# Kernel tuning notes

Measured on AMD Instinct MI355X. Metric: run time of the kernel, lower is better.

The kernel has to match this reference:

```python
import jax, jax.numpy as jnp
import numpy as np
from math import factorial as _f

MAX_L = 2
NUM_CHANNELS = 64
B, N, C = 4, 1024, 64


def _cg_coeff(l1, m1, l2, m2, L, M):
    # Standard real Clebsch-Gordan coefficient <l1 m1 l2 m2 | L M> (Condon-Shortley)
    if m1 + m2 != M or not (abs(l1 - l2) <= L <= l1 + l2):
        return 0.0
    pre = ((2 * L + 1) * _f(L + l1 - l2) * _f(L - l1 + l2) * _f(l1 + l2 - L) / _f(l1 + l2 + L + 1)) ** 0.5
    pre *= (_f(L + M) * _f(L - M) * _f(l1 - m1) * _f(l1 + m1) * _f(l2 - m2) * _f(l2 + m2)) ** 0.5
    s = 0.0
    for k in range(0, l1 + l2 - L + 1):
        dens = [k, l1 + l2 - L - k, l1 - m1 - k, l2 + m2 - k, L - l2 + m1 + k, L - l1 - m2 + k]
        if any(d < 0 for d in dens):
            continue
        term = (-1.0) ** k
        for d in dens:
            term /= _f(d)
        s += term
    return pre * s


def _cg_tensor(l1, l2, L):
    # dense CG block [2l1+1, 2l2+1, 2L+1]
    T = np.zeros((2 * l1 + 1, 2 * l2 + 1, 2 * L + 1), np.float32)
    for i, m1 in enumerate(range(-l1, l1 + 1)):
        for j, m2 in enumerate(range(-l2, l2 + 1)):
            for k, M in enumerate(range(-L, L + 1)):
                T[i, j, k] = _cg_coeff(l1, m1, l2, m2, L, M)
    return jnp.asarray(T)


# precompute small CG blocks once (tiny, static)
_CG = {(l1, l2, L): _cg_tensor(l1, l2, L)
       for l1 in range(MAX_L + 1) for l2 in range(MAX_L + 1)
       for L in range(MAX_L + 1) if abs(l1 - l2) <= L <= l1 + l2}


def setup_inputs() -> dict:
    key = jax.random.key(0)
    ks = jax.random.split(key, 7)
    inp = {}
    for l, k in zip(range(MAX_L + 1), ks[:3]):
        inp[f"v{l}"] = jax.random.normal(k, (B, N, 2 * l + 1, C), jnp.float32)
    for l, k in zip(range(MAX_L + 1), ks[3:6]):
        inp[f"s{l}"] = jax.random.normal(k, (B, N, N, 2 * l + 1, 1), jnp.float32)
    inp["conn"] = jax.random.randint(ks[6], (B, N, N), 0, 2, jnp.int32)
    return inp


def reference(v0, v1, v2, s0, s1, s2, conn):
    v = [v0, v1, v2]
    sph = [s0, s1, s2]
    # sphx.parts[l] = einsum('bijmc->bimc', sph.parts[l]) : sum over neighbor index j
    sx = [jnp.einsum('bijmc->bimc', s) for s in sph]
    adj = conn.astype(v0.dtype)  # [B,N,N] gather mask (Rmask1)

    # CGproduct(vertices, sphx): for each output degree L, concat all (l1,l2) fragments
    cg_parts = []
    for L in range(MAX_L + 1):
        frags = []
        for l1 in range(MAX_L + 1):
            for l2 in range(MAX_L + 1):
                if abs(l1 - l2) <= L <= l1 + l2:
                    # [B,N,2L+1,C*1]
                    o = jnp.einsum('bnic,bnjd,ijk->bnkcd', v[l1], sx[l2], _CG[(l1, l2, L)])
                    frags.append(o.reshape(o.shape[0], o.shape[1], 2 * L + 1, -1))
        cg_parts.append(jnp.concatenate(frags, axis=-1))

    # message passing: sum-gather over connected neighbors
    mp = [jnp.einsum('bnm,bmkc->bnkc', adj, p) for p in cg_parts]

    # per-l normalization: divide by (2l+1)*||part||_F / num_channels
    normed = []
    for L, p in enumerate(mp):
        nf = (2 * L + 1) * jnp.linalg.norm(p)
        normed.append(p / (nf / NUM_CHANNELS))

    # flatten (m, channel) per degree and concat for a single output array
    return jnp.concatenate([p.reshape(p.shape[0], p.shape[1], -1) for p in normed], axis=-1)
```

## Files before the change

### kernel.cpp

```cpp
#include <hip/hip_runtime.h>
#include <math.h>

typedef __attribute__((ext_vector_type(8))) short short8;
typedef __attribute__((ext_vector_type(4))) float f32x4;

#define B_   4
#define N_   1024
#define FTOT 3264
#define FPAD 3328

#define WS_SS   0
#define WS_CG   256
#define WS_SX   4096
#define WS_ABF  151552
#define WS_PT   8540160

__device__ __forceinline__ unsigned short f2bf(float x) {
  union { float f; unsigned u; } v; v.f = x;
  unsigned r = v.u + 0x7FFFu + ((v.u >> 16) & 1u);
  return (unsigned short)(r >> 16);
}

__device__ __forceinline__ void gload16(const void* gp, void* lp) {
  __builtin_amdgcn_global_load_lds((const __attribute__((address_space(1))) unsigned int*)gp,
                                   (__attribute__((address_space(3))) unsigned int*)lp, 16, 0, 0);
}

__device__ __forceinline__ float wave_sum(float v) {
#pragma unroll
  for (int off = 32; off > 0; off >>= 1) v += __shfl_down(v, off, 64);
  return v;
}

__device__ double dfact(int n) { double r = 1.0; for (int i = 2; i <= n; ++i) r *= (double)i; return r; }

__device__ float cg_coeff(int l1, int m1, int l2, int m2, int L, int M) {
  if (m1 + m2 != M) return 0.f;
  int dl = l1 - l2; if (dl < 0) dl = -dl;
  if (L < dl || L > l1 + l2) return 0.f;
  double pre = sqrt((double)(2*L+1) * dfact(L+l1-l2) * dfact(L-l1+l2) * dfact(l1+l2-L) / dfact(l1+l2+L+1));
  pre *= sqrt(dfact(L+M)*dfact(L-M)*dfact(l1-m1)*dfact(l1+m1)*dfact(l2-m2)*dfact(l2+m2));
  double s = 0.0;
  for (int k = 0; k <= l1 + l2 - L; ++k) {
    int d1 = l1+l2-L-k, d2 = l1-m1-k, d3 = l2+m2-k, d4 = L-l2+m1+k, d5 = L-l1-m2+k;
    if (d1 < 0 || d2 < 0 || d3 < 0 || d4 < 0 || d5 < 0) continue;
    double t = (k & 1) ? -1.0 : 1.0;
    t /= dfact(k)*dfact(d1)*dfact(d2)*dfact(d3)*dfact(d4)*dfact(d5);
    s += t;
  }
  return (float)(pre * s);
}

__device__ const int t_l1[15]  = {0,1,2, 0,1,1,1,2,2, 0,1,1,2,2,2};
__device__ const int t_l2[15]  = {0,1,2, 1,0,1,2,1,2, 2,1,2,0,1,2};
__device__ const int t_L [15]  = {0,0,0, 1,1,1,1,1,1, 2,2,2,2,2,2};
__device__ const int t_off[16] = {0,1,10, 35,44,53,80,125,170, 245,270,315,390,415,490, 615};

__device__ const int d_l1[3][6]  = {{0,1,2,0,0,0},{0,1,1,1,2,2},{0,1,1,2,2,2}};
__device__ const int d_l2[3][6]  = {{0,1,2,0,0,0},{1,0,1,2,1,2},{2,1,2,0,1,2}};
__device__ const int d_off[3][6] = {{0,1,10,0,0,0},{35,44,53,80,125,170},{245,270,315,390,415,490}};
__device__ const int d_rb[3] = {0, 1, 4};


__global__ void k_init(float* ss, float* cg) {
  int tid = threadIdx.x;
  if (tid < 4) ss[tid] = 0.f;
  if (tid >= 615) return;
  int t = 0;
  while (t < 14 && tid >= t_off[t+1]) ++t;
  int local = tid - t_off[t];
  int l1 = t_l1[t], l2 = t_l2[t], L = t_L[t];
  int nk = 2*L+1, n2 = 2*l2+1;
  int k = local % nk; int rest = local / nk;
  int j = rest % n2;  int i = rest / n2;
  cg[tid] = cg_coeff(l1, i - l1, l2, j - l2, L, k - L);
}

__global__ __launch_bounds__(256) void k_sx(const float* __restrict__ s0p, const float* __restrict__ s1p,
                                            const float* __restrict__ s2p, float* __restrict__ sx) {
  __shared__ float red[9][256];
  const int bn = blockIdx.x;
  const int tid = threadIdx.x;
  const float* p0 = s0p + (size_t)bn * 1024;
  const float* p1 = s1p + (size_t)bn * 3072;
  const float* p2 = s2p + (size_t)bn * 5120;
  float a0 = 0.f;
  for (int i = tid; i < 1024; i += 256) a0 += p0[i];
  float b0 = 0.f, b1 = 0.f, b2 = 0.f;
  for (int i = tid; i < 3072; i += 768) { b0 += p1[i]; b1 += p1[i+256]; b2 += p1[i+512]; }
  float c0=0.f,c1=0.f,c2=0.f,c3=0.f,c4=0.f;
  for (int i = tid; i < 5120; i += 1280) {
    c0 += p2[i]; c1 += p2[i+256]; c2 += p2[i+512]; c3 += p2[i+768]; c4 += p2[i+1024];
  }
  red[0][tid] = a0;
  const int r3 = tid % 3;
  red[1 + r3][tid]        = b0;
  red[1 + (r3+1)%3][tid]  = b1;
  red[1 + (r3+2)%3][tid]  = b2;
  const int r5 = tid % 5;
  red[4 + r5][tid]        = c0;
  red[4 + (r5+1)%5][tid]  = c1;
  red[4 + (r5+2)%5][tid]  = c2;
  red[4 + (r5+3)%5][tid]  = c3;
  red[4 + (r5+4)%5][tid]  = c4;
  __syncthreads();
  for (int s = 128; s > 0; s >>= 1) {
    if (tid < s) {
#pragma unroll
      for (int r = 0; r < 9; ++r) red[r][tid] += red[r][tid + s];
    }
    __syncthreads();
  }
  if (tid < 9) sx[(size_t)bn * 9 + tid] = red[tid][0];
}

__global__ __launch_bounds__(256) void k_adj(const int* __restrict__ conn, unsigned short* __restrict__ Abf) {
  const int idx  = blockIdx.x * 256 + threadIdx.x;
  const int lane = idx & 63;
  const int w    = (idx >> 6) & 2047;
  const int b    = idx >> 17;
  const int nt16 = w >> 5;
  const int ks   = w & 31;
  const int l16  = lane & 15, quad = lane >> 4;
  const int n    = nt16 * 16 + l16;
  const int m8   = ks * 32 + quad * 8;
  const int4* src = (const int4*)(conn + ((size_t)(b * 1024 + n) * 1024 + m8));
  int4 c0 = src[0], c1 = src[1];
  short8 o;
  o[0] = f2bf((float)c0.x); o[1] = f2bf((float)c0.y);
  o[2] = f2bf((float)c0.z); o[3] = f2bf((float)c0.w);
  o[4] = f2bf((float)c1.x); o[5] = f2bf((float)c1.y);
  o[6] = f2bf((float)c1.z); o[7] = f2bf((float)c1.w);
  const int nt = n >> 7, nr = n & 127;
  *(short8*)&Abf[(size_t)(b * 8 + nt) * 131072 + ks * 4096 +
                 ((nr >> 4) * 4 + quad) * 128 + (nr & 15) * 8] = o;
}

#define VSTRIDE 148

template <int L>
__device__ __forceinline__ void cg_emit(const float* __restrict__ vme, const float sxr[9],
                                        const float* __restrict__ cgt,
                                        unsigned short* __restrict__ pout, int cbase) {
  const int nfrag = (L == 0) ? 3 : 6;
  const int nk = 2 * L + 1;
  const int Lbase = (L == 0) ? 0 : (L == 1 ? 192 : 1344);
  const int Cfrag = nfrag * 64;
#pragma unroll
  for (int frag = 0; frag < nfrag; ++frag) {
    const int l1 = d_l1[L][frag], l2 = d_l2[L][frag];
    const int n1 = 2 * l1 + 1, n2 = 2 * l2 + 1;
    const int rb1 = d_rb[l1], rb2 = d_rb[l2];
    const int cgo = d_off[L][frag];
#pragma unroll
    for (int k = 0; k < nk; ++k) {
      float w[5];
#pragma unroll
      for (int i = 0; i < n1; ++i) {
        float a = 0.f;
#pragma unroll
        for (int j = 0; j < n2; ++j)
          a += sxr[rb2 + j] * cgt[cgo + (i * n2 + j) * nk + k];
        w[i] = a;
      }
      f32x4 val = {0.f, 0.f, 0.f, 0.f};
#pragma unroll
      for (int i = 0; i < n1; ++i) {
        f32x4 vv = *(const f32x4*)(vme + (rb1 + i) * 16);
        val += vv * w[i];
      }
      const int fb = Lbase + k * Cfrag + frag * 64 + cbase;
      const int ftile = fb >> 7, fr = fb & 127;
      unsigned short* pp = pout + (size_t)ftile * 131072 + (fr >> 4) * 512 + (fr & 15) * 8;
#pragma unroll
      for (int cc = 0; cc < 4; ++cc)
        pp[cc * 8] = f2bf(val[cc]);
    }
  }
}

__global__ __launch_bounds__(256) void k_cgp(const float* __restrict__ v0, const float* __restrict__ v1,
                                             const float* __restrict__ v2, const float* __restrict__ sx,
                                             const float* __restrict__ cgt, unsigned short* __restrict__ Pt) {
  __shared__ float vsh[64 * VSTRIDE];
  const int half = blockIdx.x & 1;
  const int cq   = blockIdx.x >> 1;
  const int mt   = blockIdx.y;
  const int b    = blockIdx.z;
  const int m0 = mt * 64;
  const int c0 = cq * 16;
  const int tid = threadIdx.x;
  const size_t nb = (size_t)b * N_ + m0;

  for (int e = tid; e < 9216; e += 256) {
    const int m = e / 144, rest = e % 144;
    const int r = rest >> 4, cc = rest & 15;
    float val;
    if (r == 0)      val = v0[(nb + m) * 64 + c0 + cc];
    else if (r < 4)  val = v1[((nb + m) * 3 + (r - 1)) * 64 + c0 + cc];
    else             val = v2[((nb + m) * 5 + (r - 4)) * 64 + c0 + cc];
    vsh[m * VSTRIDE + rest] = val;
  }
  const int lane = tid & 63, wv = tid >> 6;
  float sxr[9];
#pragma unroll
  for (int r = 0; r < 9; ++r) sxr[r] = sx[(nb + lane) * 9 + r];
  __syncthreads();

  const int ks = mt * 2 + (lane >> 5);
  const int kq = ((lane & 31) >> 3) * 128 + (lane & 7);
  unsigned short* pout = Pt + (size_t)b * 26 * 131072 + ks * 4096 + kq;
  const int cbase = c0 + wv * 4;
  const float* vme = &vsh[lane * VSTRIDE + wv * 4];

  if (half == 0) {
    cg_emit<0>(vme, sxr, cgt, pout, cbase);
    cg_emit<1>(vme, sxr, cgt, pout, cbase);
  } else {
    cg_emit<2>(vme, sxr, cgt, pout, cbase);
    const int fr = 64 + cbase;
    unsigned short* pp = pout + (size_t)25 * 131072 + (fr >> 4) * 512 + (fr & 15) * 8;
#pragma unroll
    for (int cc = 0; cc < 4; ++cc)
      pp[cc * 8] = 0;
  }
}

#define WAIT_VM8 0x0F78
#define WAIT_VM0 0x0F70

__global__ __launch_bounds__(256) void k_gemm(const unsigned short* __restrict__ PtT,
                                              const unsigned short* __restrict__ AbT,
                                              float* __restrict__ out, float* __restrict__ ssv) {
  __shared__ unsigned short As[2][8192];
  __shared__ unsigned short Bs[2][8192];
  const int i  = blockIdx.x;
  const int x  = i & 7, j = i >> 3;
  const int b  = j / 26;
  const int r  = j % 26;
  const int ft = (x >> 2) * 13 + (r % 13);
  const int nt = (x & 3) * 2 + (r / 13);
  const int f0 = ft * 128, n0 = nt * 128;
  const int tid  = threadIdx.x;
  const int wid  = tid >> 6, lane = tid & 63;
  const int wr   = wid >> 1, wc = wid & 1;
  const int l16  = lane & 15, quad = lane >> 4;

  const unsigned short* gA = PtT + (size_t)(b * 26 + ft) * 131072 + wid * 2048 + lane * 8;
  const unsigned short* gB = AbT + (size_t)(b * 8  + nt) * 131072 + wid * 2048 + lane * 8;

#define ISSUE(S, BUF) do { \
    const unsigned short* a_ = gA + (S) * 8192; \
    const unsigned short* b_ = gB + (S) * 8192; \
    unsigned short* la_ = &As[BUF][wid * 2048]; \
    unsigned short* lb_ = &Bs[BUF][wid * 2048]; \
    gload16(a_,        la_);        gload16(a_ +  512, la_ +  512); \
    gload16(a_ + 1024, la_ + 1024); gload16(a_ + 1536, la_ + 1536); \
    gload16(b_,        lb_);        gload16(b_ +  512, lb_ +  512); \
    gload16(b_ + 1024, lb_ + 1024); gload16(b_ + 1536, lb_ + 1536); \
  } while (0)

  f32x4 acc[4][4] = {};

#define COMPUTE(BUF) do { \
    _Pragma("unroll") \
    for (int kc = 0; kc < 2; ++kc) { \
      short8 af[4], bf[4]; \
      _Pragma("unroll") \
      for (int mi = 0; mi < 4; ++mi) \
        af[mi] = *(const short8*)&As[BUF][kc*4096 + (wr*4+mi)*512 + quad*128 + l16*8]; \
      _Pragma("unroll") \
      for (int ni = 0; ni < 4; ++ni) \
        bf[ni] = *(const short8*)&Bs[BUF][kc*4096 + (wc*4+ni)*512 + quad*128 + l16*8]; \
      _Pragma("unroll") \
      for (int mi = 0; mi < 4; ++mi) \
        _Pragma("unroll") \
        for (int ni = 0; ni < 4; ++ni) \
          acc[mi][ni] = __builtin_amdgcn_mfma_f32_16x16x32_bf16(af[mi], bf[ni], acc[mi][ni], 0, 0, 0); \
    } \
  } while (0)

  ISSUE(0, 0);
  ISSUE(1, 1);
  for (int s = 0; s < 15; ++s) {
    const int buf = s & 1;
    __builtin_amdgcn_s_waitcnt(WAIT_VM8);
    __builtin_amdgcn_s_barrier();
    COMPUTE(buf);
    __builtin_amdgcn_s_barrier();
    if (s < 14) ISSUE(s + 2, buf);
  }
  __builtin_amdgcn_s_waitcnt(WAIT_VM0);
  __builtin_amdgcn_s_barrier();
  COMPUTE(1);

  float ssl0 = 0.f, ssl1 = 0.f, ssl2 = 0.f;
#pragma unroll
  for (int mi = 0; mi < 4; ++mi) {
    const int fbase = f0 + wr*64 + mi*16 + quad*4;
    if (fbase >= FTOT) continue;
    float sq = 0.f;
#pragma unroll
    for (int ni = 0; ni < 4; ++ni) {
      const int n = n0 + wc*64 + ni*16 + l16;
      f32x4 v = acc[mi][ni];
      sq += v[0]*v[0] + v[1]*v[1] + v[2]*v[2] + v[3]*v[3];
      *(f32x4*)&out[((size_t)b * N_ + n) * FTOT + fbase] = v;
    }
    if (fbase < 192) ssl0 += sq; else if (fbase < 1344) ssl1 += sq; else ssl2 += sq;
  }
  ssl0 = wave_sum(ssl0); ssl1 = wave_sum(ssl1); ssl2 = wave_sum(ssl2);
  if (lane == 0) {
    if (ssl0 != 0.f) atomicAdd(&ssv[0], ssl0);
    if (ssl1 != 0.f) atomicAdd(&ssv[1], ssl1);
    if (ssl2 != 0.f) atomicAdd(&ssv[2], ssl2);
  }
#undef ISSUE
#undef COMPUTE
}

__global__ __launch_bounds__(256) void k_scale(float* __restrict__ out, const float* __restrict__ ssv) {
  const int idx = blockIdx.x * 256 + threadIdx.x;
  const int total = B_ * N_ * (FTOT / 4);
  if (idx >= total) return;
  const int f = (idx % (FTOT / 4)) * 4;
  const int L = f < 192 ? 0 : (f < 1344 ? 1 : 2);
  const float sc = 64.f / ((float)(2*L+1) * sqrtf(ssv[L]));
  f32x4* p = (f32x4*)out + idx;
  f32x4 v = *p;
  v *= sc;
  *p = v;
}

extern "C" void kernel_launch(void* const* d_in, const int* in_sizes, int n_in,
                              void* d_out, int out_size, void* d_ws, size_t ws_size,
                              hipStream_t stream) {
  const float* v0 = (const float*)d_in[0];
  const float* v1 = (const float*)d_in[1];
  const float* v2 = (const float*)d_in[2];
  const float* s0 = (const float*)d_in[3];
  const float* s1 = (const float*)d_in[4];
  const float* s2 = (const float*)d_in[5];
  const int* conn = (const int*)d_in[6];
  char* ws = (char*)d_ws;
  float* ss            = (float*)(ws + WS_SS);
  float* cg            = (float*)(ws + WS_CG);
  float* sx            = (float*)(ws + WS_SX);
  unsigned short* Abf  = (unsigned short*)(ws + WS_ABF);
  unsigned short* Pt   = (unsigned short*)(ws + WS_PT);
  float* out = (float*)d_out;

  k_init <<<dim3(1),            dim3(640), 0, stream>>>(ss, cg);
  k_sx   <<<dim3(B_ * N_),      dim3(256), 0, stream>>>(s0, s1, s2, sx);
  k_adj  <<<dim3(2048),         dim3(256), 0, stream>>>(conn, Abf);
  k_cgp  <<<dim3(8, 16, B_),    dim3(256), 0, stream>>>(v0, v1, v2, sx, cg, Pt);
  k_gemm <<<dim3(832),          dim3(256), 0, stream>>>(Pt, Abf, out, ss);
  k_scale<<<dim3(13056),        dim3(256), 0, stream>>>(out, ss);
}
```

Measured before the change: 329.2 us.

## Enlarge GEMM tile to 256x256 with 8 waves per block

The GEMM kernel moves from 128x128 tiles with 4 waves to 256x256 tiles with 8 waves (512 threads), so each wave computes 128x64 outputs and more data is reused per LDS load. The grid shrinks from 832 to 208 blocks, and the block-to-tile mapping now groups the four batch tiles' work differently. Per-wave norm partial sums are reduced in shared memory before one atomic per degree per block. The cost is a larger LDS footprint (64KB), more accumulator registers, and only 208 blocks on a 256-CU device, which may leave CUs idle.

Result: faster. 299.8 us (-8.9%).

```diff
diff --git a/kernel.cpp b/kernel.cpp
--- a/kernel.cpp
+++ b/kernel.cpp
@@ -229,66 +229,75 @@
 #define WAIT_VM8 0x0F78
 #define WAIT_VM0 0x0F70
 
-__global__ __launch_bounds__(256) void k_gemm(const unsigned short* __restrict__ PtT,
-                                              const unsigned short* __restrict__ AbT,
-                                              float* __restrict__ out, float* __restrict__ ssv) {
-  __shared__ unsigned short As[2][8192];
-  __shared__ unsigned short Bs[2][8192];
+__global__ __launch_bounds__(512, 2) void k_gemm(const unsigned short* __restrict__ PtT,
+                                                 const unsigned short* __restrict__ AbT,
+                                                 float* __restrict__ out, float* __restrict__ ssv) {
+  __shared__ unsigned short As[2][2][8192];
+  __shared__ unsigned short Bs[2][2][8192];
   const int i  = blockIdx.x;
   const int x  = i & 7, j = i >> 3;
-  const int b  = j / 26;
-  const int r  = j % 26;
-  const int ft = (x >> 2) * 13 + (r % 13);
-  const int nt = (x & 3) * 2 + (r / 13);
-  const int f0 = ft * 128, n0 = nt * 128;
+  const int b   = x >> 1;
+  const int ntp = 2 * (x & 1) + (j & 1);
+  const int ftp = j >> 1;
+  const int f0 = ftp * 256, n0 = ntp * 256;
   const int tid  = threadIdx.x;
-  const int wid  = tid >> 6, lane = tid & 63;
-  const int wr   = wid >> 1, wc = wid & 1;
+  const int w    = tid >> 6, lane = tid & 63;
+  const int wr   = w >> 2, wc = w & 3;
   const int l16  = lane & 15, quad = lane >> 4;
 
-  const unsigned short* gA = PtT + (size_t)(b * 26 + ft) * 131072 + wid * 2048 + lane * 8;
-  const unsigned short* gB = AbT + (size_t)(b * 8  + nt) * 131072 + wid * 2048 + lane * 8;
-
-#define ISSUE(S, BUF) do { \
-    const unsigned short* a_ = gA + (S) * 8192; \
-    const unsigned short* b_ = gB + (S) * 8192; \
-    unsigned short* la_ = &As[BUF][wid * 2048]; \
-    unsigned short* lb_ = &Bs[BUF][wid * 2048]; \
-    gload16(a_,        la_);        gload16(a_ +  512, la_ +  512); \
-    gload16(a_ + 1024, la_ + 1024); gload16(a_ + 1536, la_ + 1536); \
-    gload16(b_,        lb_);        gload16(b_ +  512, lb_ +  512); \
-    gload16(b_ + 1024, lb_ + 1024); gload16(b_ + 1536, lb_ + 1536); \
+  const unsigned short* gA0 = PtT + (size_t)(b * 26 + 2 * ftp    ) * 131072;
+  const unsigned short* gA1 = PtT + (size_t)(b * 26 + 2 * ftp + 1) * 131072;
+  const unsigned short* gB0 = AbT + (size_t)(b * 8  + 2 * ntp    ) * 131072;
+  const unsigned short* gB1 = AbT + (size_t)(b * 8  + 2 * ntp + 1) * 131072;
+  const int so = w * 512 + lane * 8;
+
+#define ISSUE(T, BUF) do { \
+    const size_t o = (size_t)(T) * 8192 + so; \
+    gload16(gA0 + o,        &As[BUF][0][w * 512]); \
+    gload16(gA0 + o + 4096, &As[BUF][0][4096 + w * 512]); \
+    gload16(gA1 + o,        &As[BUF][1][w * 512]); \
+    gload16(gA1 + o + 4096, &As[BUF][1][4096 + w * 512]); \
+    gload16(gB0 + o,        &Bs[BUF][0][w * 512]); \
+    gload16(gB0 + o + 4096, &Bs[BUF][0][4096 + w * 512]); \
+    gload16(gB1 + o,        &Bs[BUF][1][w * 512]); \
+    gload16(gB1 + o + 4096, &Bs[BUF][1][4096 + w * 512]); \
   } while (0)
 
-  f32x4 acc[4][4] = {};
+  f32x4 acc[8][4] = {};
+  const int bh  = wc >> 1;
+  const int bl4 = (wc & 1) * 4;
 
 #define COMPUTE(BUF) do { \
     _Pragma("unroll") \
     for (int kc = 0; kc < 2; ++kc) { \
-      short8 af[4], bf[4]; \
-      _Pragma("unroll") \
-      for (int mi = 0; mi < 4; ++mi) \
-        af[mi] = *(const short8*)&As[BUF][kc*4096 + (wr*4+mi)*512 + quad*128 + l16*8]; \
+      short8 bf[4]; \
       _Pragma("unroll") \
       for (int ni = 0; ni < 4; ++ni) \
-        bf[ni] = *(const short8*)&Bs[BUF][kc*4096 + (wc*4+ni)*512 + quad*128 + l16*8]; \
+        bf[ni] = *(const short8*)&Bs[BUF][bh][kc*4096 + ((bl4 + ni)*4 + quad)*128 + l16*8]; \
       _Pragma("unroll") \
-      for (int mi = 0; mi < 4; ++mi) \
+      for (int mh = 0; mh < 2; ++mh) { \
+        short8 af[4]; \
         _Pragma("unroll") \
-        for (int ni = 0; ni < 4; ++ni) \
-          acc[mi][ni] = __builtin_amdgcn_mfma_f32_16x16x32_bf16(af[mi], bf[ni], acc[mi][ni], 0, 0, 0); \
+        for (int m = 0; m < 4; ++m) \
+          af[m] = *(const short8*)&As[BUF][wr][kc*4096 + ((mh*4 + m)*4 + quad)*128 + l16*8]; \
+        _Pragma("unroll") \
+        for (int m = 0; m < 4; ++m) \
+          _Pragma("unroll") \
+          for (int ni = 0; ni < 4; ++ni) \
+            acc[mh*4 + m][ni] = __builtin_amdgcn_mfma_f32_16x16x32_bf16(af[m], bf[ni], acc[mh*4 + m][ni], 0, 0, 0); \
+      } \
     } \
   } while (0)
 
   ISSUE(0, 0);
   ISSUE(1, 1);
-  for (int s = 0; s < 15; ++s) {
-    const int buf = s & 1;
+  for (int t = 0; t < 15; ++t) {
+    const int buf = t & 1;
     __builtin_amdgcn_s_waitcnt(WAIT_VM8);
     __builtin_amdgcn_s_barrier();
     COMPUTE(buf);
     __builtin_amdgcn_s_barrier();
-    if (s < 14) ISSUE(s + 2, buf);
+    if (t < 14) ISSUE(t + 2, buf);
   }
   __builtin_amdgcn_s_waitcnt(WAIT_VM0);
   __builtin_amdgcn_s_barrier();
@@ -296,8 +305,8 @@
 
   float ssl0 = 0.f, ssl1 = 0.f, ssl2 = 0.f;
 #pragma unroll
-  for (int mi = 0; mi < 4; ++mi) {
-    const int fbase = f0 + wr*64 + mi*16 + quad*4;
+  for (int mi = 0; mi < 8; ++mi) {
+    const int fbase = f0 + wr*128 + mi*16 + quad*4;
     if (fbase >= FTOT) continue;
     float sq = 0.f;
 #pragma unroll
@@ -310,10 +319,16 @@
     if (fbase < 192) ssl0 += sq; else if (fbase < 1344) ssl1 += sq; else ssl2 += sq;
   }
   ssl0 = wave_sum(ssl0); ssl1 = wave_sum(ssl1); ssl2 = wave_sum(ssl2);
-  if (lane == 0) {
-    if (ssl0 != 0.f) atomicAdd(&ssv[0], ssl0);
-    if (ssl1 != 0.f) atomicAdd(&ssv[1], ssl1);
-    if (ssl2 != 0.f) atomicAdd(&ssv[2], ssl2);
+
+  __syncthreads();
+  float* red = (float*)&As[0][0][0];
+  if (lane == 0) { red[w*3 + 0] = ssl0; red[w*3 + 1] = ssl1; red[w*3 + 2] = ssl2; }
+  __syncthreads();
+  if (tid < 3) {
+    float s = 0.f;
+#pragma unroll
+    for (int ww = 0; ww < 8; ++ww) s += red[ww*3 + tid];
+    if (s != 0.f) atomicAdd(&ssv[tid], s);
   }
 #undef ISSUE
 #undef COMPUTE
@@ -354,6 +369,6 @@
   k_sx   <<<dim3(B_ * N_),      dim3(256), 0, stream>>>(s0, s1, s2, sx);
   k_adj  <<<dim3(2048),         dim3(256), 0, stream>>>(conn, Abf);
   k_cgp  <<<dim3(8, 16, B_),    dim3(256), 0, stream>>>(v0, v1, v2, sx, cg, Pt);
-  k_gemm <<<dim3(832),          dim3(256), 0, stream>>>(Pt, Abf, out, ss);
+  k_gemm <<<dim3(208),          dim3(512), 0, stream>>>(Pt, Abf, out, ss);
   k_scale<<<dim3(13056),        dim3(256), 0, stream>>>(out, ss);
 }
```
